# Performance work log

Measured on AMD Instinct MI355X. Metric: run time of the kernel, lower is better.

The kernel has to match this reference:

```python
import jax, jax.numpy as jnp
import numpy as np

B, C, H, W, K = 64, 64, 32, 32, 1024  # C == dim_dict, K == size_dict
BETA = 0.25


def setup_inputs() -> dict:
    key = jax.random.key(0)
    k1, k2, k3 = jax.random.split(key, 3)
    return {
        "z_from_encoder": jax.random.normal(k1, (B, C, H, W), dtype=jnp.float32),
        "codebook": jax.random.normal(k2, (K, C), dtype=jnp.float32),
        "codebook_weight": jax.random.normal(k3, (K,), dtype=jnp.float32),
        "flg_train": 1,
    }


def reference(z_from_encoder, codebook, codebook_weight, flg_train):
    # NCHW -> NHWC, flatten to (N, D)
    z = jnp.transpose(z_from_encoder, (0, 2, 3, 1))
    zf = z.reshape(-1, z.shape[-1])                      # (N, D)
    # squared euclidean distances via expansion (N, K)
    d = (jnp.sum(zf ** 2, axis=1, keepdims=True)
         + jnp.sum(codebook ** 2, axis=1)
         - 2.0 * zf @ codebook.T)
    idx = jnp.argmin(d, axis=1)                          # (N,)
    # one-hot @ codebook == gather
    z_q = codebook[idx].reshape(z.shape)                 # (B, H, W, D)
    if flg_train:
        loss = (BETA * jnp.mean((jax.lax.stop_gradient(z_q) - z) ** 2)
                + jnp.mean((z_q - jax.lax.stop_gradient(z)) ** 2))
    else:
        loss = jnp.float32(0.0)
    # straight-through estimator
    z_q_st = z + jax.lax.stop_gradient(z_q - z)
    # codebook usage histogram -> perplexity
    n_tok = zf.shape[0]
    e_mean = jnp.zeros((codebook.shape[0],), z.dtype).at[idx].add(1.0) / n_tok
    perplexity = jnp.exp(-jnp.sum(e_mean * jnp.log(e_mean + 1e-10)))
    z_q_out = jnp.transpose(z_q_st, (0, 3, 1, 2))        # back to NCHW
    return z_q_out, loss, perplexity
```

## Files before the change

kernel.cpp:

```cpp
#include <hip/hip_runtime.h>


typedef __attribute__((ext_vector_type(8))) short short8;
typedef __attribute__((ext_vector_type(4))) float float4v;

#define NELEM 4194304

#define WS_CBF   0
#define WS_C2H   262144
#define WS_HIST  266240
#define WS_LOSS  270336

__device__ __forceinline__ unsigned bf16_rne(float x) {
    unsigned u = __float_as_uint(x);
    return (u + 0x7fffu + ((u >> 16) & 1u)) >> 16;
}

__global__ __launch_bounds__(256) void prep_kernel(
    const float* __restrict__ cb, ushort* __restrict__ cbf,
    float* __restrict__ c2h, int* __restrict__ hist, float* __restrict__ loss_part) {
    __shared__ float s_c2[2][16];
    int tid  = threadIdx.x;
    int lane = tid & 63, wave = tid >> 6;
    int quad = lane >> 4, col = lane & 15;
    int bx   = blockIdx.x;

    if (bx >= 64) {
        hist[(bx - 64) * 256 + tid] = 0;
        if (bx == 64 && tid < 64) loss_part[tid] = 0.f;
        return;
    }
    int c = bx, fid = wave;
    int st = fid & 1, split = fid >> 1;
    int code  = c * 16 + col;
    int dbase = st * 32 + quad * 8;
    const float* cp = cb + code * 64 + dbase;
    float4v v0 = *(const float4v*)cp;
    float4v v1 = *(const float4v*)(cp + 4);
    float xs[8] = {v0.x, v0.y, v0.z, v0.w, v1.x, v1.y, v1.z, v1.w};
    short8 frag;
    float ssq = 0.f;
#pragma unroll
    for (int j = 0; j < 8; j++) {
        float x = xs[j];
        ssq = fmaf(x, x, ssq);
        unsigned hb = bf16_rne(x);
        if (split == 0) frag[j] = (short)hb;
        else            frag[j] = (short)bf16_rne(x - __uint_as_float(hb << 16));
    }
    *(short8*)(cbf + ((c * 4 + fid) * 64 + lane) * 8) = frag;
    if (split == 0) {
        ssq += __shfl_xor(ssq, 16);
        ssq += __shfl_xor(ssq, 32);
        if (quad == 0) s_c2[st][col] = ssq;
    }
    __syncthreads();
    if (tid < 16) c2h[c * 16 + tid] = -0.5f * (s_c2[0][tid] + s_c2[1][tid]);
}

__global__ __launch_bounds__(256, 4) void vq_kernel(
    const float* __restrict__ z, const float* __restrict__ cb,
    const ushort* __restrict__ cbf, const float* __restrict__ c2h,
    float* __restrict__ out, float* __restrict__ loss_part, int* __restrict__ hist)
{
    __shared__ float s_q[64 * 65];
    __shared__ float s_ms[2][64];
    __shared__ int   s_mi[2][64];
    __shared__ int   s_idx[64];
    __shared__ float s_red[4];

    int tid  = threadIdx.x;
    int lane = tid & 63, wave = tid >> 6;
    int quad = lane >> 4, col = lane & 15;
    int bx   = blockIdx.x;

    int tokbase = bx * 64;
    int bb = tokbase >> 10, hwb = tokbase & 1023;
    const float* zb = z + bb * 65536 + hwb;
    int tokhalf = wave & 1, khalf = wave >> 1;

    short8 ah[2][2], al[2][2];
#pragma unroll
    for (int g = 0; g < 2; g++) {
        int rel = tokhalf * 32 + g * 16 + col;
#pragma unroll
        for (int st = 0; st < 2; st++) {
            short8 h8, l8;
#pragma unroll
            for (int j = 0; j < 8; j++) {
                int d = st * 32 + quad * 8 + j;
                float x = zb[d * 1024 + rel];
                unsigned hb = bf16_rne(x);
                h8[j] = (short)hb;
                l8[j] = (short)bf16_rne(x - __uint_as_float(hb << 16));
            }
            ah[g][st] = h8; al[g][st] = l8;
        }
    }

    float best[2][4]; int bidx[2][4];
#pragma unroll
    for (int g = 0; g < 2; g++)
#pragma unroll
        for (int r = 0; r < 4; r++) { best[g][r] = -1e38f; bidx[g][r] = 0; }

    int cbase = khalf * 32;
    const ushort* cw = cbf + lane * 8;
    {
        const ushort* p0 = cw + cbase * 2048;
        short8 nb0 = *(const short8*)(p0 + 0);
        short8 nb1 = *(const short8*)(p0 + 512);
        short8 nb2 = *(const short8*)(p0 + 1024);
        short8 nb3 = *(const short8*)(p0 + 1536);
        float  nini = c2h[cbase * 16 + col];
        for (int cc = 0; cc < 32; cc++) {
            short8 bh0 = nb0, bh1 = nb1, bl0 = nb2, bl1 = nb3;
            float  ini = nini;
            if (cc < 31) {
                const ushort* np = cw + (cbase + cc + 1) * 2048;
                nb0 = *(const short8*)(np + 0);
                nb1 = *(const short8*)(np + 512);
                nb2 = *(const short8*)(np + 1024);
                nb3 = *(const short8*)(np + 1536);
                nini = c2h[(cbase + cc + 1) * 16 + col];
            }
            int code = (cbase + cc) * 16 + col;
#pragma unroll
            for (int g = 0; g < 2; g++) {
                float4v a0 = {ini, ini, ini, ini};
                float4v a1 = {0.f, 0.f, 0.f, 0.f};
                a0 = __builtin_amdgcn_mfma_f32_16x16x32_bf16(ah[g][0], bh0, a0, 0, 0, 0);
                a1 = __builtin_amdgcn_mfma_f32_16x16x32_bf16(ah[g][1], bh1, a1, 0, 0, 0);
                a0 = __builtin_amdgcn_mfma_f32_16x16x32_bf16(ah[g][0], bl0, a0, 0, 0, 0);
                a1 = __builtin_amdgcn_mfma_f32_16x16x32_bf16(ah[g][1], bl1, a1, 0, 0, 0);
                a0 = __builtin_amdgcn_mfma_f32_16x16x32_bf16(al[g][0], bh0, a0, 0, 0, 0);
                a1 = __builtin_amdgcn_mfma_f32_16x16x32_bf16(al[g][1], bh1, a1, 0, 0, 0);
                a0 = __builtin_amdgcn_mfma_f32_16x16x32_bf16(al[g][0], bl0, a0, 0, 0, 0);
                a1 = __builtin_amdgcn_mfma_f32_16x16x32_bf16(al[g][1], bl1, a1, 0, 0, 0);
#pragma unroll
                for (int r = 0; r < 4; r++) {
                    float s = a0[r] + a1[r];
                    if (s > best[g][r]) { best[g][r] = s; bidx[g][r] = code; }
                }
            }
        }
    }

#pragma unroll
    for (int g = 0; g < 2; g++) {
#pragma unroll
        for (int r = 0; r < 4; r++) {
            float s = best[g][r]; int ix = bidx[g][r];
#pragma unroll
            for (int m = 1; m <= 8; m <<= 1) {
                float so = __shfl_xor(s, m);
                int   io = __shfl_xor(ix, m);
                if (so > s || (so == s && io < ix)) { s = so; ix = io; }
            }
            if (col == 0) {
                int t = tokhalf * 32 + g * 16 + quad * 4 + r;
                s_ms[khalf][t] = s; s_mi[khalf][t] = ix;
            }
        }
    }
    __syncthreads();

    if (tid < 64) {
        float s0 = s_ms[0][tid], s1 = s_ms[1][tid];
        int   i0 = s_mi[0][tid], i1 = s_mi[1][tid];
        int   ix = (s1 > s0) ? i1 : i0;
        s_idx[tid] = ix;
        atomicAdd(&hist[ix], 1);
    }
    __syncthreads();

#pragma unroll
    for (int p = 0; p < 16; p++) {
        int i = p * 256 + tid;
        int t = i >> 6, d = i & 63;
        s_q[t * 65 + d] = cb[s_idx[t] * 64 + d];
    }
    __syncthreads();

    float ls = 0.f;
#pragma unroll 4
    for (int p = 0; p < 16; p++) {
        int i = p * 256 + tid;
        int d = i >> 6, t = i & 63;
        int a = d * 1024 + t;
        float zv = zb[a];
        float q  = s_q[t * 65 + d];
        float df = q - zv;
        out[bb * 65536 + hwb + a] = zv + df;
        ls = fmaf(df, df, ls);
    }
#pragma unroll
    for (int off = 32; off; off >>= 1) ls += __shfl_down(ls, off);
    if (lane == 0) s_red[wave] = ls;
    __syncthreads();
    if (tid == 0) {
        float v = (s_red[0] + s_red[1]) + (s_red[2] + s_red[3]);
        atomicAdd(&loss_part[bx & 63], v);
    }
}

__global__ __launch_bounds__(1024) void finalize_kernel(
    const int* __restrict__ hist, const float* __restrict__ loss_part,
    const int* __restrict__ flg, float* __restrict__ out) {
    __shared__ float red[16];
    int   k = threadIdx.x;
    float e = (float)hist[k] * (1.0f / 65536.0f);
    float v = e * logf(e + 1e-10f);
#pragma unroll
    for (int off = 32; off; off >>= 1) v += __shfl_down(v, off);
    if ((k & 63) == 0) red[k >> 6] = v;
    __syncthreads();
    if (k == 0) {
        float s = 0.f;
#pragma unroll
        for (int i = 0; i < 16; i++) s += red[i];
        out[NELEM + 1] = expf(-s);

        float ls = 0.f;
        for (int i = 0; i < 64; i++) ls += loss_part[i];
        float m    = ls * (1.0f / (float)NELEM);
        out[NELEM] = (*flg) ? (0.25f * m + m) : 0.0f;
    }
}

extern "C" void kernel_launch(void* const* d_in, const int* in_sizes, int n_in,
                              void* d_out, int out_size, void* d_ws, size_t ws_size,
                              hipStream_t stream) {
    const float* z   = (const float*)d_in[0];
    const float* cb  = (const float*)d_in[1];
    const int*   flg = (const int*)d_in[3];

    float* out = (float*)d_out;
    char*  ws  = (char*)d_ws;

    ushort* cbf       = (ushort*)(ws + WS_CBF);
    float*  c2h       = (float*)(ws + WS_C2H);
    int*    hist      = (int*)(ws + WS_HIST);
    float*  loss_part = (float*)(ws + WS_LOSS);

    prep_kernel<<<68, 256, 0, stream>>>(cb, cbf, c2h, hist, loss_part);
    vq_kernel<<<1024, 256, 0, stream>>>(z, cb, cbf, c2h, out, loss_part, hist);
    finalize_kernel<<<1, 1024, 0, stream>>>(hist, loss_part, flg, out);
}
```

Measured before the change: 122.4 us.

## Drop low*low MFMA term, split codes across waves, fuse finalize via last-block

Each wave now handles all 64 tokens of the block and a quarter of the codebook. It drops the al*bl MFMA term, so each distance uses six MFMAs instead of eight, and the double-buffered codebook prefetch is removed. The separate finalize kernel is folded into vq_kernel through an atomic done-counter, with the last block computing perplexity and loss, which saves one kernel launch. Dropping the low*low term slightly lowers distance precision and could flip near-tie argmins. Register pressure rises (launch bounds go from 4 to 3 waves per SIMD).

```diff
diff --git a/kernel.cpp b/kernel.cpp
--- a/kernel.cpp
+++ b/kernel.cpp
@@ -5,11 +5,13 @@
 typedef __attribute__((ext_vector_type(4))) float float4v;
 
 #define NELEM 4194304
+#define NBLK  1024
 
 #define WS_CBF   0
 #define WS_C2H   262144
 #define WS_HIST  266240
 #define WS_LOSS  270336
+#define WS_DONE  270592
 
 __device__ __forceinline__ unsigned bf16_rne(float x) {
     unsigned u = __float_as_uint(x);
@@ -18,7 +20,8 @@
 
 __global__ __launch_bounds__(256) void prep_kernel(
     const float* __restrict__ cb, ushort* __restrict__ cbf,
-    float* __restrict__ c2h, int* __restrict__ hist, float* __restrict__ loss_part) {
+    float* __restrict__ c2h, int* __restrict__ hist,
+    float* __restrict__ loss_part, int* __restrict__ done) {
     __shared__ float s_c2[2][16];
     int tid  = threadIdx.x;
     int lane = tid & 63, wave = tid >> 6;
@@ -28,6 +31,7 @@
     if (bx >= 64) {
         hist[(bx - 64) * 256 + tid] = 0;
         if (bx == 64 && tid < 64) loss_part[tid] = 0.f;
+        if (bx == 64 && tid == 64) *done = 0;
         return;
     }
     int c = bx, fid = wave;
@@ -58,16 +62,18 @@
     if (tid < 16) c2h[c * 16 + tid] = -0.5f * (s_c2[0][tid] + s_c2[1][tid]);
 }
 
-__global__ __launch_bounds__(256, 4) void vq_kernel(
+__global__ __launch_bounds__(256, 3) void vq_kernel(
     const float* __restrict__ z, const float* __restrict__ cb,
     const ushort* __restrict__ cbf, const float* __restrict__ c2h,
-    float* __restrict__ out, float* __restrict__ loss_part, int* __restrict__ hist)
+    const int* __restrict__ flg, float* __restrict__ out,
+    float* __restrict__ loss_part, int* __restrict__ hist, int* __restrict__ done)
 {
     __shared__ float s_q[64 * 65];
-    __shared__ float s_ms[2][64];
-    __shared__ int   s_mi[2][64];
+    __shared__ float s_ms[4][64];
+    __shared__ int   s_mi[4][64];
     __shared__ int   s_idx[64];
     __shared__ float s_red[4];
+    __shared__ int   s_last;
 
     int tid  = threadIdx.x;
     int lane = tid & 63, wave = tid >> 6;
@@ -77,12 +83,11 @@
     int tokbase = bx * 64;
     int bb = tokbase >> 10, hwb = tokbase & 1023;
     const float* zb = z + bb * 65536 + hwb;
-    int tokhalf = wave & 1, khalf = wave >> 1;
-
-    short8 ah[2][2], al[2][2];
-#pragma unroll
-    for (int g = 0; g < 2; g++) {
-        int rel = tokhalf * 32 + g * 16 + col;
+
+    short8 ah[4][2], al[4][2];
+#pragma unroll
+    for (int g = 0; g < 4; g++) {
+        int rel = g * 16 + col;
 #pragma unroll
         for (int st = 0; st < 2; st++) {
             short8 h8, l8;
@@ -98,56 +103,40 @@
         }
     }
 
-    float best[2][4]; int bidx[2][4];
-#pragma unroll
-    for (int g = 0; g < 2; g++)
+    float best[4][4]; int bidx[4][4];
+#pragma unroll
+    for (int g = 0; g < 4; g++)
 #pragma unroll
         for (int r = 0; r < 4; r++) { best[g][r] = -1e38f; bidx[g][r] = 0; }
 
-    int cbase = khalf * 32;
     const ushort* cw = cbf + lane * 8;
-    {
-        const ushort* p0 = cw + cbase * 2048;
-        short8 nb0 = *(const short8*)(p0 + 0);
-        short8 nb1 = *(const short8*)(p0 + 512);
-        short8 nb2 = *(const short8*)(p0 + 1024);
-        short8 nb3 = *(const short8*)(p0 + 1536);
-        float  nini = c2h[cbase * 16 + col];
-        for (int cc = 0; cc < 32; cc++) {
-            short8 bh0 = nb0, bh1 = nb1, bl0 = nb2, bl1 = nb3;
-            float  ini = nini;
-            if (cc < 31) {
-                const ushort* np = cw + (cbase + cc + 1) * 2048;
-                nb0 = *(const short8*)(np + 0);
-                nb1 = *(const short8*)(np + 512);
-                nb2 = *(const short8*)(np + 1024);
-                nb3 = *(const short8*)(np + 1536);
-                nini = c2h[(cbase + cc + 1) * 16 + col];
-            }
-            int code = (cbase + cc) * 16 + col;
-#pragma unroll
-            for (int g = 0; g < 2; g++) {
-                float4v a0 = {ini, ini, ini, ini};
-                float4v a1 = {0.f, 0.f, 0.f, 0.f};
-                a0 = __builtin_amdgcn_mfma_f32_16x16x32_bf16(ah[g][0], bh0, a0, 0, 0, 0);
-                a1 = __builtin_amdgcn_mfma_f32_16x16x32_bf16(ah[g][1], bh1, a1, 0, 0, 0);
-                a0 = __builtin_amdgcn_mfma_f32_16x16x32_bf16(ah[g][0], bl0, a0, 0, 0, 0);
-                a1 = __builtin_amdgcn_mfma_f32_16x16x32_bf16(ah[g][1], bl1, a1, 0, 0, 0);
-                a0 = __builtin_amdgcn_mfma_f32_16x16x32_bf16(al[g][0], bh0, a0, 0, 0, 0);
-                a1 = __builtin_amdgcn_mfma_f32_16x16x32_bf16(al[g][1], bh1, a1, 0, 0, 0);
-                a0 = __builtin_amdgcn_mfma_f32_16x16x32_bf16(al[g][0], bl0, a0, 0, 0, 0);
-                a1 = __builtin_amdgcn_mfma_f32_16x16x32_bf16(al[g][1], bl1, a1, 0, 0, 0);
-#pragma unroll
-                for (int r = 0; r < 4; r++) {
-                    float s = a0[r] + a1[r];
-                    if (s > best[g][r]) { best[g][r] = s; bidx[g][r] = code; }
-                }
-            }
-        }
-    }
-
-#pragma unroll
-    for (int g = 0; g < 2; g++) {
+    for (int cc = 0; cc < 16; cc++) {
+        int ch = (wave << 4) + cc;
+        const ushort* p = cw + ch * 2048;
+        short8 bh0 = *(const short8*)(p + 0);
+        short8 bh1 = *(const short8*)(p + 512);
+        short8 bl0 = *(const short8*)(p + 1024);
+        short8 bl1 = *(const short8*)(p + 1536);
+        float  ini = c2h[ch * 16 + col];
+        int   code = ch * 16 + col;
+#pragma unroll
+        for (int g = 0; g < 4; g++) {
+            float4v acc = {ini, ini, ini, ini};
+            acc = __builtin_amdgcn_mfma_f32_16x16x32_bf16(ah[g][0], bh0, acc, 0, 0, 0);
+            acc = __builtin_amdgcn_mfma_f32_16x16x32_bf16(ah[g][1], bh1, acc, 0, 0, 0);
+            acc = __builtin_amdgcn_mfma_f32_16x16x32_bf16(ah[g][0], bl0, acc, 0, 0, 0);
+            acc = __builtin_amdgcn_mfma_f32_16x16x32_bf16(ah[g][1], bl1, acc, 0, 0, 0);
+            acc = __builtin_amdgcn_mfma_f32_16x16x32_bf16(al[g][0], bh0, acc, 0, 0, 0);
+            acc = __builtin_amdgcn_mfma_f32_16x16x32_bf16(al[g][1], bh1, acc, 0, 0, 0);
+#pragma unroll
+            for (int r = 0; r < 4; r++) {
+                if (acc[r] > best[g][r]) { best[g][r] = acc[r]; bidx[g][r] = code; }
+            }
+        }
+    }
+
+#pragma unroll
+    for (int g = 0; g < 4; g++) {
 #pragma unroll
         for (int r = 0; r < 4; r++) {
             float s = best[g][r]; int ix = bidx[g][r];
@@ -158,19 +147,22 @@
                 if (so > s || (so == s && io < ix)) { s = so; ix = io; }
             }
             if (col == 0) {
-                int t = tokhalf * 32 + g * 16 + quad * 4 + r;
-                s_ms[khalf][t] = s; s_mi[khalf][t] = ix;
+                int t = g * 16 + quad * 4 + r;
+                s_ms[wave][t] = s; s_mi[wave][t] = ix;
             }
         }
     }
     __syncthreads();
 
     if (tid < 64) {
-        float s0 = s_ms[0][tid], s1 = s_ms[1][tid];
-        int   i0 = s_mi[0][tid], i1 = s_mi[1][tid];
-        int   ix = (s1 > s0) ? i1 : i0;
-        s_idx[tid] = ix;
-        atomicAdd(&hist[ix], 1);
+        float sb = s_ms[0][tid]; int ib = s_mi[0][tid];
+#pragma unroll
+        for (int q = 1; q < 4; q++) {
+            float sq_ = s_ms[q][tid];
+            if (sq_ > sb) { sb = sq_; ib = s_mi[q][tid]; }
+        }
+        s_idx[tid] = ib;
+        atomicAdd(&hist[ib], 1);
     }
     __syncthreads();
 
@@ -201,30 +193,34 @@
     if (tid == 0) {
         float v = (s_red[0] + s_red[1]) + (s_red[2] + s_red[3]);
         atomicAdd(&loss_part[bx & 63], v);
-    }
-}
-
-__global__ __launch_bounds__(1024) void finalize_kernel(
-    const int* __restrict__ hist, const float* __restrict__ loss_part,
-    const int* __restrict__ flg, float* __restrict__ out) {
-    __shared__ float red[16];
-    int   k = threadIdx.x;
-    float e = (float)hist[k] * (1.0f / 65536.0f);
-    float v = e * logf(e + 1e-10f);
-#pragma unroll
-    for (int off = 32; off; off >>= 1) v += __shfl_down(v, off);
-    if ((k & 63) == 0) red[k >> 6] = v;
-    __syncthreads();
-    if (k == 0) {
-        float s = 0.f;
-#pragma unroll
-        for (int i = 0; i < 16; i++) s += red[i];
-        out[NELEM + 1] = expf(-s);
-
-        float ls = 0.f;
-        for (int i = 0; i < 64; i++) ls += loss_part[i];
-        float m    = ls * (1.0f / (float)NELEM);
-        out[NELEM] = (*flg) ? (0.25f * m + m) : 0.0f;
+        __threadfence();
+        s_last = (atomicAdd(done, 1) == NBLK - 1);
+    }
+    __syncthreads();
+
+    if (s_last) {
+        float v = 0.f;
+#pragma unroll
+        for (int i = 0; i < 4; i++) {
+            int h = atomicAdd(&hist[tid * 4 + i], 0);
+            float e = (float)h * (1.0f / 65536.0f);
+            v += e * logf(e + 1e-10f);
+        }
+#pragma unroll
+        for (int off = 32; off; off >>= 1) v += __shfl_down(v, off);
+        if (lane == 0) s_red[wave] = v;
+        __syncthreads();
+        if (tid < 64) {
+            float lv = atomicAdd(&loss_part[tid], 0.f);
+#pragma unroll
+            for (int off = 32; off; off >>= 1) lv += __shfl_down(lv, off);
+            if (tid == 0) {
+                float ent = (s_red[0] + s_red[1]) + (s_red[2] + s_red[3]);
+                out[NELEM + 1] = expf(-ent);
+                float m = lv * (1.0f / (float)NELEM);
+                out[NELEM] = (*flg) ? (0.25f * m + m) : 0.0f;
+            }
+        }
     }
 }
 
@@ -242,8 +238,8 @@
     float*  c2h       = (float*)(ws + WS_C2H);
     int*    hist      = (int*)(ws + WS_HIST);
     float*  loss_part = (float*)(ws + WS_LOSS);
-
-    prep_kernel<<<68, 256, 0, stream>>>(cb, cbf, c2h, hist, loss_part);
-    vq_kernel<<<1024, 256, 0, stream>>>(z, cb, cbf, c2h, out, loss_part, hist);
-    finalize_kernel<<<1, 1024, 0, stream>>>(hist, loss_part, flg, out);
-}
+    int*    done      = (int*)(ws + WS_DONE);
+
+    prep_kernel<<<68, 256, 0, stream>>>(cb, cbf, c2h, hist, loss_part, done);
+    vq_kernel<<<NBLK, 256, 0, stream>>>(z, cb, cbf, c2h, flg, out, loss_part, hist, done);
+}
```

Measured after the change: 155.7 us. +27.2%, slower.

## Split VQ into argmin and elementwise output kernels, drop lo*lo MFMA term

Applied to the files above, without the earlier changes.

Splits the fused kernel in two. An argmin kernel has each wave cover all 64 tokens against a quarter of the codebook, and a separate vectorised output kernel gathers codebook values to write the straight-through output and loss partials. The split-bf16 product loses its low*low term, cutting six MFMAs to six per group instead of eight, and the argmin kernel needs no shared staging buffer. The cost is an extra launch, an index round-trip through global memory and z being read twice. Dropping the lo*lo term slightly lowers distance precision and could flip near-tie argmins.

```diff
diff --git a/kernel.cpp b/kernel.cpp
--- a/kernel.cpp
+++ b/kernel.cpp
@@ -10,6 +10,7 @@
 #define WS_C2H   262144
 #define WS_HIST  266240
 #define WS_LOSS  270336
+#define WS_IDX   270592
 
 __device__ __forceinline__ unsigned bf16_rne(float x) {
     unsigned u = __float_as_uint(x);
@@ -58,16 +59,12 @@
     if (tid < 16) c2h[c * 16 + tid] = -0.5f * (s_c2[0][tid] + s_c2[1][tid]);
 }
 
-__global__ __launch_bounds__(256, 4) void vq_kernel(
-    const float* __restrict__ z, const float* __restrict__ cb,
-    const ushort* __restrict__ cbf, const float* __restrict__ c2h,
-    float* __restrict__ out, float* __restrict__ loss_part, int* __restrict__ hist)
+__global__ __launch_bounds__(256, 3) void argmin_kernel(
+    const float* __restrict__ z, const ushort* __restrict__ cbf,
+    const float* __restrict__ c2h, int* __restrict__ idx_out, int* __restrict__ hist)
 {
-    __shared__ float s_q[64 * 65];
-    __shared__ float s_ms[2][64];
-    __shared__ int   s_mi[2][64];
-    __shared__ int   s_idx[64];
-    __shared__ float s_red[4];
+    __shared__ float s_ms[4][64];
+    __shared__ int   s_mi[4][64];
 
     int tid  = threadIdx.x;
     int lane = tid & 63, wave = tid >> 6;
@@ -77,12 +74,11 @@
     int tokbase = bx * 64;
     int bb = tokbase >> 10, hwb = tokbase & 1023;
     const float* zb = z + bb * 65536 + hwb;
-    int tokhalf = wave & 1, khalf = wave >> 1;
-
-    short8 ah[2][2], al[2][2];
-#pragma unroll
-    for (int g = 0; g < 2; g++) {
-        int rel = tokhalf * 32 + g * 16 + col;
+
+    short8 ah[4][2], al[4][2];
+#pragma unroll
+    for (int g = 0; g < 4; g++) {
+        int rel = g * 16 + col;
 #pragma unroll
         for (int st = 0; st < 2; st++) {
             short8 h8, l8;
@@ -98,13 +94,13 @@
         }
     }
 
-    float best[2][4]; int bidx[2][4];
-#pragma unroll
-    for (int g = 0; g < 2; g++)
+    float best[4][4]; int bidx[4][4];
+#pragma unroll
+    for (int g = 0; g < 4; g++)
 #pragma unroll
         for (int r = 0; r < 4; r++) { best[g][r] = -1e38f; bidx[g][r] = 0; }
 
-    int cbase = khalf * 32;
+    int cbase = wave << 4;
     const ushort* cw = cbf + lane * 8;
     {
         const ushort* p0 = cw + cbase * 2048;
@@ -113,10 +109,10 @@
         short8 nb2 = *(const short8*)(p0 + 1024);
         short8 nb3 = *(const short8*)(p0 + 1536);
         float  nini = c2h[cbase * 16 + col];
-        for (int cc = 0; cc < 32; cc++) {
+        for (int cc = 0; cc < 16; cc++) {
             short8 bh0 = nb0, bh1 = nb1, bl0 = nb2, bl1 = nb3;
             float  ini = nini;
-            if (cc < 31) {
+            if (cc < 15) {
                 const ushort* np = cw + (cbase + cc + 1) * 2048;
                 nb0 = *(const short8*)(np + 0);
                 nb1 = *(const short8*)(np + 512);
@@ -126,28 +122,24 @@
             }
             int code = (cbase + cc) * 16 + col;
 #pragma unroll
-            for (int g = 0; g < 2; g++) {
-                float4v a0 = {ini, ini, ini, ini};
-                float4v a1 = {0.f, 0.f, 0.f, 0.f};
-                a0 = __builtin_amdgcn_mfma_f32_16x16x32_bf16(ah[g][0], bh0, a0, 0, 0, 0);
-                a1 = __builtin_amdgcn_mfma_f32_16x16x32_bf16(ah[g][1], bh1, a1, 0, 0, 0);
-                a0 = __builtin_amdgcn_mfma_f32_16x16x32_bf16(ah[g][0], bl0, a0, 0, 0, 0);
-                a1 = __builtin_amdgcn_mfma_f32_16x16x32_bf16(ah[g][1], bl1, a1, 0, 0, 0);
-                a0 = __builtin_amdgcn_mfma_f32_16x16x32_bf16(al[g][0], bh0, a0, 0, 0, 0);
-                a1 = __builtin_amdgcn_mfma_f32_16x16x32_bf16(al[g][1], bh1, a1, 0, 0, 0);
-                a0 = __builtin_amdgcn_mfma_f32_16x16x32_bf16(al[g][0], bl0, a0, 0, 0, 0);
-                a1 = __builtin_amdgcn_mfma_f32_16x16x32_bf16(al[g][1], bl1, a1, 0, 0, 0);
+            for (int g = 0; g < 4; g++) {
+                float4v acc = {ini, ini, ini, ini};
+                acc = __builtin_amdgcn_mfma_f32_16x16x32_bf16(ah[g][0], bh0, acc, 0, 0, 0);
+                acc = __builtin_amdgcn_mfma_f32_16x16x32_bf16(ah[g][1], bh1, acc, 0, 0, 0);
+                acc = __builtin_amdgcn_mfma_f32_16x16x32_bf16(ah[g][0], bl0, acc, 0, 0, 0);
+                acc = __builtin_amdgcn_mfma_f32_16x16x32_bf16(ah[g][1], bl1, acc, 0, 0, 0);
+                acc = __builtin_amdgcn_mfma_f32_16x16x32_bf16(al[g][0], bh0, acc, 0, 0, 0);
+                acc = __builtin_amdgcn_mfma_f32_16x16x32_bf16(al[g][1], bh1, acc, 0, 0, 0);
 #pragma unroll
                 for (int r = 0; r < 4; r++) {
-                    float s = a0[r] + a1[r];
-                    if (s > best[g][r]) { best[g][r] = s; bidx[g][r] = code; }
+                    if (acc[r] > best[g][r]) { best[g][r] = acc[r]; bidx[g][r] = code; }
                 }
             }
         }
     }
 
 #pragma unroll
-    for (int g = 0; g < 2; g++) {
+    for (int g = 0; g < 4; g++) {
 #pragma unroll
         for (int r = 0; r < 4; r++) {
             float s = best[g][r]; int ix = bidx[g][r];
@@ -158,49 +150,56 @@
                 if (so > s || (so == s && io < ix)) { s = so; ix = io; }
             }
             if (col == 0) {
-                int t = tokhalf * 32 + g * 16 + quad * 4 + r;
-                s_ms[khalf][t] = s; s_mi[khalf][t] = ix;
+                int t = g * 16 + quad * 4 + r;
+                s_ms[wave][t] = s; s_mi[wave][t] = ix;
             }
         }
     }
     __syncthreads();
 
     if (tid < 64) {
-        float s0 = s_ms[0][tid], s1 = s_ms[1][tid];
-        int   i0 = s_mi[0][tid], i1 = s_mi[1][tid];
-        int   ix = (s1 > s0) ? i1 : i0;
-        s_idx[tid] = ix;
-        atomicAdd(&hist[ix], 1);
-    }
-    __syncthreads();
-
-#pragma unroll
-    for (int p = 0; p < 16; p++) {
-        int i = p * 256 + tid;
-        int t = i >> 6, d = i & 63;
-        s_q[t * 65 + d] = cb[s_idx[t] * 64 + d];
-    }
-    __syncthreads();
-
-    float ls = 0.f;
-#pragma unroll 4
-    for (int p = 0; p < 16; p++) {
-        int i = p * 256 + tid;
-        int d = i >> 6, t = i & 63;
-        int a = d * 1024 + t;
-        float zv = zb[a];
-        float q  = s_q[t * 65 + d];
-        float df = q - zv;
-        out[bb * 65536 + hwb + a] = zv + df;
-        ls = fmaf(df, df, ls);
-    }
+        float sb = s_ms[0][tid]; int ib = s_mi[0][tid];
+#pragma unroll
+        for (int q = 1; q < 4; q++) {
+            float sq_ = s_ms[q][tid];
+            if (sq_ > sb) { sb = sq_; ib = s_mi[q][tid]; }
+        }
+        idx_out[tokbase + tid] = ib;
+        atomicAdd(&hist[ib], 1);
+    }
+}
+
+__global__ __launch_bounds__(256) void output_kernel(
+    const float* __restrict__ z, const float* __restrict__ cb,
+    const int* __restrict__ idx, float* __restrict__ out,
+    float* __restrict__ loss_part)
+{
+    __shared__ float s_red[4];
+    int tid = threadIdx.x;
+    int i   = blockIdx.x * 256 + tid;
+    int e0  = i * 4;
+    int hw0 = e0 & 1023;
+    int t   = e0 >> 10;
+    int c   = t & 63, b = t >> 6;
+
+    int4   iv = *(const int4*)(idx + b * 1024 + hw0);
+    float4 zv = *(const float4*)(z + e0);
+    float q0 = cb[iv.x * 64 + c];
+    float q1 = cb[iv.y * 64 + c];
+    float q2 = cb[iv.z * 64 + c];
+    float q3 = cb[iv.w * 64 + c];
+    float d0 = q0 - zv.x, d1 = q1 - zv.y, d2 = q2 - zv.z, d3 = q3 - zv.w;
+    float4 ov = {zv.x + d0, zv.y + d1, zv.z + d2, zv.w + d3};
+    *(float4*)(((float*)out) + e0) = ov;
+
+    float ls = (d0 * d0 + d1 * d1) + (d2 * d2 + d3 * d3);
 #pragma unroll
     for (int off = 32; off; off >>= 1) ls += __shfl_down(ls, off);
-    if (lane == 0) s_red[wave] = ls;
+    if ((tid & 63) == 0) s_red[tid >> 6] = ls;
     __syncthreads();
     if (tid == 0) {
         float v = (s_red[0] + s_red[1]) + (s_red[2] + s_red[3]);
-        atomicAdd(&loss_part[bx & 63], v);
+        atomicAdd(&loss_part[blockIdx.x & 63], v);
     }
 }
 
@@ -242,8 +241,10 @@
     float*  c2h       = (float*)(ws + WS_C2H);
     int*    hist      = (int*)(ws + WS_HIST);
     float*  loss_part = (float*)(ws + WS_LOSS);
+    int*    idx       = (int*)(ws + WS_IDX);
 
     prep_kernel<<<68, 256, 0, stream>>>(cb, cbf, c2h, hist, loss_part);
-    vq_kernel<<<1024, 256, 0, stream>>>(z, cb, cbf, c2h, out, loss_part, hist);
+    argmin_kernel<<<1024, 256, 0, stream>>>(z, cbf, c2h, idx, hist);
+    output_kernel<<<4096, 256, 0, stream>>>(z, cb, idx, out, loss_part);
     finalize_kernel<<<1, 1024, 0, stream>>>(hist, loss_part, flg, out);
 }
```

New measurement: 150.0 us. 1.23x slower.
